# Optimization experiments

Hardware: AMD Instinct MI355X
Metric: run time of the kernel (lower is better)

The kernel has to match this reference:

```python
import jax, jax.numpy as jnp
import numpy as np

IN_CH, OUT_CH, KS = 64, 128, 3
GRID, DEG = 8, 3
STRIDE, PAD = 1, 1
SIZE = IN_CH * KS * KS            # 576
NCOEF = GRID + DEG                # 11
GRID_RANGE = (-1.0, 1.0)


def _xavier_uniform(key, shape):
    fan_out, fan_in = shape
    a = float(np.sqrt(6.0 / (fan_in + fan_out)))
    return jax.random.uniform(key, shape, minval=-a, maxval=a, dtype=jnp.float32)


def setup_inputs() -> dict:
    key = jax.random.key(0)
    k1, k2, k3 = jax.random.split(key, 3)
    x = jax.random.normal(k1, (8, IN_CH, 32, 32), dtype=jnp.float32)
    # non-trainable knot grid, one row per unfolded feature
    knots = jnp.tile(jnp.linspace(GRID_RANGE[0], GRID_RANGE[1], GRID + 1, dtype=jnp.float32)[None, :], (SIZE, 1))
    coeff = 0.1 * jax.random.normal(k2, (OUT_CH, SIZE, NCOEF), dtype=jnp.float32)
    base_weights = _xavier_uniform(k3, (OUT_CH, SIZE))
    spline_weights = jnp.ones((OUT_CH, SIZE), dtype=jnp.float32)
    return {"x": x, "knots": knots, "coeff": coeff,
            "base_weights": base_weights, "spline_weights": spline_weights}


def bspline_basis(x, grid, k):
    # x: (S, P) evaluation points; grid: (S, G+1) knots. Returns (S, G+k, P).
    h = (grid[:, -1:] - grid[:, :1]) / (grid.shape[1] - 1)
    left = grid[:, :1] - h * jnp.arange(k, 0, -1, dtype=x.dtype)
    right = grid[:, -1:] + h * jnp.arange(1, k + 1, dtype=x.dtype)
    g = jnp.concatenate([left, grid, right], axis=1)  # (S, G+1+2k)
    xe = x[:, None, :]
    B = ((xe >= g[:, :-1, None]) & (xe < g[:, 1:, None])).astype(x.dtype)
    for d in range(1, k + 1):  # de Boor recursion over fixed degree
        B = ((xe - g[:, :-(d + 1), None]) / (g[:, d:-1, None] - g[:, :-(d + 1), None]) * B[:, :-1]
             + (g[:, d + 1:, None] - xe) / (g[:, d + 1:, None] - g[:, 1:-d, None]) * B[:, 1:])
    return B


def _unfold(x):
    # torch F.unfold with channel-major (c, kh, kw) feature ordering
    N, C, H, W = x.shape
    xp = jnp.pad(x, ((0, 0), (0, 0), (PAD, PAD), (PAD, PAD)))
    Hp = (H + 2 * PAD - KS) // STRIDE + 1
    Wp = (W + 2 * PAD - KS) // STRIDE + 1
    patches = jnp.stack([xp[:, :, i:i + STRIDE * Hp:STRIDE, j:j + STRIDE * Wp:STRIDE]
                         for i in range(KS) for j in range(KS)], axis=2)  # (N, C, KS*KS, Hp, Wp)
    L = Hp * Wp
    u = patches.reshape(N, SIZE, L)              # (N, size, L)
    u = jnp.transpose(u, (1, 0, 2)).reshape(SIZE, N * L)  # (size, N*L), col = n*L + l
    return u, Hp, Wp


def reference(x, knots, coeff, base_weights, spline_weights):
    N = x.shape[0]
    u, Hp, Wp = _unfold(x)                                   # (size, P)
    base = base_weights @ jax.nn.silu(u)                     # (Cout, P)
    B = bspline_basis(u, knots, DEG)                         # (size, ncoef, P)
    eff = spline_weights[:, :, None] * coeff                 # (Cout, size, ncoef)
    spl = jnp.einsum('csj,sjp->cp', eff, B)                  # (Cout, P)
    out = (base + spl).reshape(OUT_CH, N, Hp, Wp)
    return jnp.transpose(out, (1, 0, 2, 3))                  # (N, Cout, Hp, Wp)
```

## Files before the change

### kernel.cpp

```cpp
#include <hip/hip_runtime.h>


typedef __attribute__((ext_vector_type(8))) short bf16x8;
typedef __attribute__((ext_vector_type(4))) float f32x4;
typedef __attribute__((ext_vector_type(16))) float f32x16;
typedef __attribute__((ext_vector_type(4))) unsigned short u16x4;

#define WSWZ_BYTES 1769472
#define PHI_OFF    WSWZ_BYTES
#define PHI_BYTES  14205696

__device__ __forceinline__ short f2bf(float f) {
    union { float f; unsigned u; } c; c.f = f;
    unsigned r = c.u + 0x7fffu + ((c.u >> 16) & 1u);
    return (short)(r >> 16);
}
__device__ __forceinline__ float bf2f(unsigned short u) {
    union { unsigned u; float f; } c; c.u = ((unsigned)u) << 16;
    return c.f;
}

__global__ void kan_prep(const float* __restrict__ coeff,
                         const float* __restrict__ basew,
                         const float* __restrict__ splw,
                         const float* __restrict__ x,
                         short* __restrict__ Wswz,
                         short* __restrict__ Phi) {
    __shared__ float coeffL[6336];
    __shared__ float basewL[576];
    __shared__ float splwL[576];
    __shared__ unsigned short xs[64 * 32];
    const int t = threadIdx.x;

    if (blockIdx.x < 272) {
        const int rowid = blockIdx.x;
        const int n     = rowid / 34;
        const int ypad  = rowid - n * 34;
        const int y     = ypad - 1;
        const bool yvalid = (y >= 0 && y < 32);

        if (yvalid) {
#pragma unroll
            for (int it = 0; it < 2; ++it) {
                int cg = t + it * 256;
                int ci = cg >> 3, q = cg & 7;
                f32x4 v = *(const f32x4*)(x + (((n * 64 + ci) * 32 + y) * 32 + q * 4));
                u16x4 p;
                p.x = (unsigned short)f2bf(v.x); p.y = (unsigned short)f2bf(v.y);
                p.z = (unsigned short)f2bf(v.z); p.w = (unsigned short)f2bf(v.w);
                *(u16x4*)&xs[ci * 32 + q * 4] = p;
            }
        }
        __syncthreads();

        const size_t rowbase = (size_t)rowid * 12 * 2176;
        for (int it = t; it < 272; it += 256) {
            int xp = it >> 3, cch = it & 7, c0 = cch << 3;
            bool interior = yvalid && (xp >= 1 && xp <= 32);
            int px = xp - 1;
            int pxc = px < 0 ? 0 : (px > 31 ? 31 : px);
            bf16x8 packs[12];
#pragma unroll
            for (int j = 0; j < 8; ++j) {
                float v = interior ? bf2f(xs[(c0 + j) * 32 + pxc]) : 0.f;
                float tt = 4.f * v + 7.f;
                int   i0 = -100;
                float b0 = 0.f, b1 = 0.f, b2 = 0.f, b3 = 0.f;
                if (tt >= 0.f && tt < 14.f) {
                    i0 = (int)tt;
                    float fr  = tt - (float)i0;
                    float omf = 1.f - fr;
                    float fr2 = fr * fr, fr3 = fr2 * fr;
                    b0 = omf * omf * omf * (1.f / 6.f);
                    b1 = (3.f * fr3 - 6.f * fr2 + 4.f) * (1.f / 6.f);
                    b2 = (-3.f * fr3 + 3.f * fr2 + 3.f * fr + 1.f) * (1.f / 6.f);
                    b3 = fr3 * (1.f / 6.f);
                }
                float silu = v * __builtin_amdgcn_rcpf(1.f + __expf(-v));
                packs[0][j] = f2bf(silu);
#pragma unroll
                for (int f = 1; f < 12; ++f) {
                    int jj = f - 1;
                    float val = 0.f;
                    val = (jj == i0 - 3) ? b0 : val;
                    val = (jj == i0 - 2) ? b1 : val;
                    val = (jj == i0 - 1) ? b2 : val;
                    val = (jj == i0    ) ? b3 : val;
                    packs[f][j] = f2bf(val);
                }
            }
            int swz = (cch ^ (xp & 7)) << 3;
#pragma unroll
            for (int f = 0; f < 12; ++f)
                *(bf16x8*)&Phi[rowbase + (size_t)f * 2176 + xp * 64 + swz] = packs[f];
        }
    } else {
        const int co = blockIdx.x - 272;
        const float* crow = coeff + co * 6336;
        for (int i = t; i < 6336; i += 256) coeffL[i] = crow[i];
        for (int i = t; i < 576; i += 256) {
            basewL[i] = basew[co * 576 + i];
            splwL[i]  = splw[co * 576 + i];
        }
        __syncthreads();
        const int cb = co >> 5, lm = co & 31;
        for (int c = t; c < 864; c += 256) {
            int kk16 = c >> 1, kh = c & 1;
            int f  = kk16 / 36;
            int rm = kk16 - f * 36;
            int tap = rm >> 2, q = rm & 3;
            bf16x8 pack;
#pragma unroll
            for (int j = 0; j < 8; ++j) {
                int ci = q * 16 + kh * 8 + j;
                int s  = ci * 9 + tap;
                float v = (f == 0) ? basewL[s] : splwL[s] * coeffL[s * 11 + (f - 1)];
                pack[j] = f2bf(v);
            }
            *(bf16x8*)(Wswz + (size_t)((kk16 * 4 + cb) * 64 + kh * 32 + lm) * 8) = pack;
        }
    }
}

__global__ __launch_bounds__(512, 2)
void kan_gemm2p(const short* __restrict__ Phi,
                const short* __restrict__ Wswz,
                float* __restrict__ out) {
    __shared__ __align__(16) short Bs[2][4 * 8704];

    const int t  = threadIdx.x;
    const int w8 = t >> 6;
    const int cb = w8 & 1;
    const int fq = w8 >> 1;
    const int l  = t & 63;
    const int ln = l & 31;
    const int kh = l >> 5;

    const int ch    = blockIdx.x >> 7;
    const int ptile = blockIdx.x & 127;
    const int n     = ptile >> 4;
    const int y0    = (ptile & 15) << 1;
    const int cbg   = ch * 2 + cb;

    const char* phiB = (const char*)Phi;
    const int rowPlane = (n * 34 + y0) * 12;
    const short* Abase = Wswz + (size_t)cbg * 512 + (size_t)l * 8;

    auto stage = [&](int r, int buf) {
#pragma unroll
        for (int k = 0; k < 9; ++k) {
            int i = t + k * 512;
            if (i < 4352) {
                int sfq = i / 1088;
                int rem = i - sfq * 1088;
                int row = rem / 272;
                int m   = rem - row * 272;
                const char* s = phiB + (size_t)(rowPlane + row * 12 + sfq * 3 + r) * 4352 + m * 16;
                __builtin_amdgcn_global_load_lds(
                    (const __attribute__((address_space(1))) unsigned int*)s,
                    (__attribute__((address_space(3))) unsigned int*)((char*)&Bs[buf][0] + i * 16),
                    16, 0, 0);
            }
        }
    };

    bf16x8 ag[36];
    auto preloadA = [&](int r) {
        const int kbase = (fq * 3 + r) * 36;
#pragma unroll
        for (int g = 0; g < 36; ++g) {
            int q  = g / 9;
            int rm = g - q * 9;
            int dx = rm / 3;
            int dy = rm - dx * 3;
            ag[g] = *(const bf16x8*)(Abase + (size_t)(kbase + (dy * 3 + dx) * 4 + q) * 2048);
        }
    };

    f32x16 acc[2];
#pragma unroll
    for (int pb = 0; pb < 2; ++pb)
#pragma unroll
        for (int r = 0; r < 16; ++r)
            acc[pb][r] = 0.f;

    auto compute = [&](const short* B0) {
#pragma unroll
        for (int q = 0; q < 4; ++q) {
#pragma unroll
            for (int dx = 0; dx < 3; ++dx) {
                const int g0 = q * 9 + dx * 3;
                const int c   = q * 2 + kh;
                const int key = (ln + dx) & 7;
                const int colb = (ln + dx) * 64 + ((c ^ key) << 3);
                bf16x8 b0 = *(const bf16x8*)&B0[0 * 2176 + colb];
                bf16x8 b1 = *(const bf16x8*)&B0[1 * 2176 + colb];
                bf16x8 b2 = *(const bf16x8*)&B0[2 * 2176 + colb];
                bf16x8 b3 = *(const bf16x8*)&B0[3 * 2176 + colb];
                acc[0] = __builtin_amdgcn_mfma_f32_32x32x16_bf16(ag[g0 + 0], b0, acc[0], 0, 0, 0);
                acc[1] = __builtin_amdgcn_mfma_f32_32x32x16_bf16(ag[g0 + 0], b1, acc[1], 0, 0, 0);
                acc[0] = __builtin_amdgcn_mfma_f32_32x32x16_bf16(ag[g0 + 1], b1, acc[0], 0, 0, 0);
                acc[1] = __builtin_amdgcn_mfma_f32_32x32x16_bf16(ag[g0 + 1], b2, acc[1], 0, 0, 0);
                acc[0] = __builtin_amdgcn_mfma_f32_32x32x16_bf16(ag[g0 + 2], b2, acc[0], 0, 0, 0);
                acc[1] = __builtin_amdgcn_mfma_f32_32x32x16_bf16(ag[g0 + 2], b3, acc[1], 0, 0, 0);
            }
        }
    };

    preloadA(0);
    stage(0, 0);
    __syncthreads();

    stage(1, 1);
    compute(&Bs[0][fq * 8704]);
    preloadA(1);
    __syncthreads();

    stage(2, 0);
    compute(&Bs[1][fq * 8704]);
    preloadA(2);
    __syncthreads();

    compute(&Bs[0][fq * 8704]);

    __syncthreads();
    float* ex = (float*)&Bs[1][0];
    if (fq != 0) {
        const int slot = (fq - 1) * 2 + cb;
#pragma unroll
        for (int pb = 0; pb < 2; ++pb)
#pragma unroll
            for (int r = 0; r < 16; ++r) {
                int v = pb * 16 + r;
                ex[slot * 2048 + l * 32 + ((v + l) & 31)] = acc[pb][r];
            }
    }
    __syncthreads();
    if (fq == 0) {
#pragma unroll
        for (int s = 0; s < 3; ++s)
#pragma unroll
            for (int pb = 0; pb < 2; ++pb)
#pragma unroll
                for (int r = 0; r < 16; ++r) {
                    int v = pb * 16 + r;
                    acc[pb][r] += ex[(s * 2 + cb) * 2048 + l * 32 + ((v + l) & 31)];
                }

#pragma unroll
        for (int pb = 0; pb < 2; ++pb) {
            int y = y0 + pb;
#pragma unroll
            for (int r = 0; r < 16; ++r) {
                int row = (r & 3) + 8 * (r >> 2) + 4 * kh;
                int co  = cbg * 32 + row;
                out[((size_t)(n * 128 + co) * 32 + y) * 32 + ln] = acc[pb][r];
            }
        }
    }
}

extern "C" void kernel_launch(void* const* d_in, const int* in_sizes, int n_in,
                              void* d_out, int out_size, void* d_ws, size_t ws_size,
                              hipStream_t stream) {
    const float* x     = (const float*)d_in[0];
    const float* coeff = (const float*)d_in[2];
    const float* basew = (const float*)d_in[3];
    const float* splw  = (const float*)d_in[4];
    float* out = (float*)d_out;

    short* Wswz = (short*)d_ws;
    short* Phi  = (short*)((char*)d_ws + PHI_OFF);

    kan_prep<<<400, 256, 0, stream>>>(coeff, basew, splw, x, Wswz, Phi);
    kan_gemm2p<<<256, 512, 0, stream>>>(Phi, Wswz, out);
}
```

Before: 96.74 us.

## Split A preloads into halves interleaved with compute; parallelize final reduction

The A-operand register preload for the next K stage is split into two halves, each issued after computing two of the four q-slices, so global loads overlap MFMA work and fewer registers are waiting at once. The epilogue now has all eight waves write partials to LDS and then cooperatively sum the four fq partials and write coalesced output, instead of wave group fq==0 doing the whole reduction and store. One barrier before the epilogue is removed. This spreads epilogue work across all waves, at the cost of extra LDS traffic from the fq==0 waves.

```diff
diff --git a/kernel.cpp b/kernel.cpp
--- a/kernel.cpp
+++ b/kernel.cpp
@@ -140,11 +140,10 @@
     const int ptile = blockIdx.x & 127;
     const int n     = ptile >> 4;
     const int y0    = (ptile & 15) << 1;
-    const int cbg   = ch * 2 + cb;
 
     const char* phiB = (const char*)Phi;
     const int rowPlane = (n * 34 + y0) * 12;
-    const short* Abase = Wswz + (size_t)cbg * 512 + (size_t)l * 8;
+    const short* Abase = Wswz + (size_t)(ch * 2 + cb) * 512 + (size_t)l * 8;
 
     auto stage = [&](int r, int buf) {
 #pragma unroll
@@ -165,15 +164,16 @@
     };
 
     bf16x8 ag[36];
-    auto preloadA = [&](int r) {
+    auto preloadA = [&](int r, int h) {
         const int kbase = (fq * 3 + r) * 36;
 #pragma unroll
-        for (int g = 0; g < 36; ++g) {
-            int q  = g / 9;
-            int rm = g - q * 9;
+        for (int g = 0; g < 18; ++g) {
+            int gg = h * 18 + g;
+            int q  = gg / 9;
+            int rm = gg - q * 9;
             int dx = rm / 3;
             int dy = rm - dx * 3;
-            ag[g] = *(const bf16x8*)(Abase + (size_t)(kbase + (dy * 3 + dx) * 4 + q) * 2048);
+            ag[gg] = *(const bf16x8*)(Abase + (size_t)(kbase + (dy * 3 + dx) * 4 + q) * 2048);
         }
     };
 
@@ -184,9 +184,10 @@
         for (int r = 0; r < 16; ++r)
             acc[pb][r] = 0.f;
 
-    auto compute = [&](const short* B0) {
-#pragma unroll
-        for (int q = 0; q < 4; ++q) {
+    auto computeQ = [&](const short* B0, int qlo) {
+#pragma unroll
+        for (int qo = 0; qo < 2; ++qo) {
+            const int q = qlo + qo;
 #pragma unroll
             for (int dx = 0; dx < 3; ++dx) {
                 const int g0 = q * 9 + dx * 3;
@@ -207,56 +208,55 @@
         }
     };
 
-    preloadA(0);
+    preloadA(0, 0); preloadA(0, 1);
     stage(0, 0);
     __syncthreads();
 
     stage(1, 1);
-    compute(&Bs[0][fq * 8704]);
-    preloadA(1);
+    computeQ(&Bs[0][fq * 8704], 0);
+    preloadA(1, 0);
+    computeQ(&Bs[0][fq * 8704], 2);
+    preloadA(1, 1);
     __syncthreads();
 
     stage(2, 0);
-    compute(&Bs[1][fq * 8704]);
-    preloadA(2);
-    __syncthreads();
-
-    compute(&Bs[0][fq * 8704]);
-
-    __syncthreads();
+    computeQ(&Bs[1][fq * 8704], 0);
+    preloadA(2, 0);
+    computeQ(&Bs[1][fq * 8704], 2);
+    preloadA(2, 1);
+    __syncthreads();
+
+    computeQ(&Bs[0][fq * 8704], 0);
+    computeQ(&Bs[0][fq * 8704], 2);
+
     float* ex = (float*)&Bs[1][0];
-    if (fq != 0) {
-        const int slot = (fq - 1) * 2 + cb;
-#pragma unroll
-        for (int pb = 0; pb < 2; ++pb)
-#pragma unroll
-            for (int r = 0; r < 16; ++r) {
-                int v = pb * 16 + r;
-                ex[slot * 2048 + l * 32 + ((v + l) & 31)] = acc[pb][r];
-            }
-    }
-    __syncthreads();
-    if (fq == 0) {
-#pragma unroll
-        for (int s = 0; s < 3; ++s)
-#pragma unroll
-            for (int pb = 0; pb < 2; ++pb)
-#pragma unroll
-                for (int r = 0; r < 16; ++r) {
-                    int v = pb * 16 + r;
-                    acc[pb][r] += ex[(s * 2 + cb) * 2048 + l * 32 + ((v + l) & 31)];
-                }
-
-#pragma unroll
-        for (int pb = 0; pb < 2; ++pb) {
-            int y = y0 + pb;
-#pragma unroll
-            for (int r = 0; r < 16; ++r) {
-                int row = (r & 3) + 8 * (r >> 2) + 4 * kh;
-                int co  = cbg * 32 + row;
-                out[((size_t)(n * 128 + co) * 32 + y) * 32 + ln] = acc[pb][r];
-            }
-        }
+#pragma unroll
+    for (int pb = 0; pb < 2; ++pb)
+#pragma unroll
+        for (int r = 0; r < 16; ++r) {
+            int v = pb * 16 + r;
+            ex[w8 * 2048 + l * 32 + ((v + l) & 31)] = acc[pb][r];
+        }
+    __syncthreads();
+
+#pragma unroll
+    for (int iter = 0; iter < 8; ++iter) {
+        int o    = w8 * 512 + iter * 64 + l;
+        int cbo  = o >> 11;
+        int pb   = (o >> 10) & 1;
+        int rr   = (o >> 5) & 31;
+        int lno  = o & 31;
+        int kho  = (rr >> 2) & 1;
+        int ro   = (rr & 3) + 4 * (rr >> 3);
+        int vo   = pb * 16 + ro;
+        int lo   = kho * 32 + lno;
+        int ewd  = lo * 32 + ((vo + lo) & 31);
+        float s = ex[(0 * 2 + cbo) * 2048 + ewd]
+                + ex[(1 * 2 + cbo) * 2048 + ewd]
+                + ex[(2 * 2 + cbo) * 2048 + ewd]
+                + ex[(3 * 2 + cbo) * 2048 + ewd];
+        int co = (ch * 2 + cbo) * 32 + rr;
+        out[((size_t)(n * 128 + co) * 32 + (y0 + pb)) * 32 + lno] = s;
     }
 }
 
```

Result: no change. 95.69 us (-1.1%).
